# Kernel tuning notes

Hardware: AMD Instinct MI355X
Metric: run time of the kernel (lower is better)

Reference implementation:

```python
import jax, jax.numpy as jnp
import numpy as np


def pairwise_dist(x):
    # Euclidean cdist via the expansion trick; grad-safe sqrt (0 grad at 0, like torch).
    sq = jnp.sum(x * x, axis=1)
    d2 = sq[:, None] + sq[None, :] - 2.0 * (x @ x.T)
    d2 = jnp.maximum(d2, 0.0)
    pos = d2 > 0
    return jnp.where(pos, jnp.sqrt(jnp.where(pos, d2, 1.0)), 0.0)


def knn_mask(dist, k):
    # per-row ascending sort; skip index 0 (self), take next k neighbors
    idx = jnp.argsort(dist, axis=1)[:, 1:k + 1]            # [N, k]
    n = dist.shape[0]
    return jnp.zeros_like(dist).at[jnp.arange(n)[:, None], idx].set(1.0)


def setup_inputs() -> dict:
    key = jax.random.key(0)
    k1, k2 = jax.random.split(key)
    N, D, K = 8192, 64, 12
    latent = jax.random.normal(k1, (N, D), dtype=jnp.float32)
    latent_norm = jnp.ones((), dtype=jnp.float32)
    X = jax.random.normal(k2, (N, D), dtype=jnp.float32)
    dist_X = pairwise_dist(X)
    pair_mask_X = knn_mask(dist_X, K)
    return {"latent": latent, "latent_norm": latent_norm,
            "dist_X": dist_X, "pair_mask_X": pair_mask_X, "k": K}


def reference(latent, latent_norm, dist_X, pair_mask_X, k):
    n = latent.shape[0]
    dist_Z = pairwise_dist(latent) / latent_norm
    pair_mask_Z = knn_mask(dist_Z, k)

    mask_diff = pair_mask_Z - pair_mask_X
    matched = (n * k - jnp.sum(mask_diff != 0) * 0.5) / (n * k)

    # match_edges == 'symmetric'
    sig1 = dist_X * pair_mask_X
    sig1_2 = dist_Z * pair_mask_X
    distance1_2 = jnp.sum(jnp.square(sig1 - sig1_2))
    sig2 = dist_Z * pair_mask_Z
    sig2_1 = dist_X * pair_mask_Z
    distance2_1 = jnp.sum(jnp.square(sig2_1 - sig2))
    distance = distance1_2 + distance2_1
    return (distance, matched, distance1_2, distance2_1)
```

## Files before the change

kernel.cpp:

```cpp
#include <hip/hip_runtime.h>
#include <stdint.h>

constexpr int NPTS = 8192;
constexpr int DIM  = 64;
constexpr int KNN  = 12;

constexpr int RT = 64;
constexpr int CT = 64;
constexpr int CS = 4;
constexpr int STRIPE = NPTS / CS;
constexpr int NCHUNK = STRIPE / CT;
constexpr int AS_STRIDE = RT + 4;
constexpr int BS_STRIDE = CT + 4;

constexpr unsigned long long SENTINEL = 0xFFFFFFFFFFFFFFFFull;

__global__ void init_out(float* out) {
  if (threadIdx.x < 4) out[threadIdx.x] = 0.0f;
}

__global__ __launch_bounds__(256) void sq_kernel(const float* __restrict__ latent,
                                                 float* __restrict__ sq) {
  int i = blockIdx.x * 256 + threadIdx.x;
  const float4* p = reinterpret_cast<const float4*>(latent + (size_t)i * DIM);
  float s = 0.f;
#pragma unroll
  for (int t = 0; t < DIM / 4; ++t) {
    float4 v = p[t];
    s += v.x * v.x + v.y * v.y + v.z * v.z + v.w * v.w;
  }
  sq[i] = s;
}

__device__ __forceinline__ void topk_insert(unsigned long long cand,
                                            unsigned long long pk[KNN]) {
#pragma unroll
  for (int s = KNN - 1; s >= 0; --s) {
    bool belongs = cand < pk[s];
    bool shift = (s > 0) && (cand < pk[s - 1]);
    unsigned long long nv = shift ? pk[s - 1] : cand;
    if (belongs) pk[s] = nv;
  }
}

__global__ __launch_bounds__(256, 2) void dz_main(
    const float* __restrict__ latent, const float* __restrict__ latent_norm,
    const float* __restrict__ dist_X, const float* __restrict__ mask_X,
    const float* __restrict__ sq, unsigned long long* __restrict__ topk_ws,
    float* __restrict__ d_out) {
  __shared__ float As[DIM * AS_STRIDE];
  __shared__ float Bs[DIM * BS_STRIDE];
  __shared__ unsigned long long buf[RT * CT];
  __shared__ int   cnt[RT];
  __shared__ float thr[RT];
  __shared__ float sqA[RT];
  __shared__ float sqB[CT];
  __shared__ float red[256];

  const int tid = threadIdx.x;
  const int tile = blockIdx.x / CS;
  const int split = blockIdx.x % CS;
  const int ib = tile * RT;
  const int jb0 = split * STRIPE;

  const float invnorm = 1.0f / latent_norm[0];

#pragma unroll
  for (int i = 0; i < (RT * DIM) / 256; ++i) {
    int flat = i * 256 + tid;
    int k = flat & (DIM - 1);
    int r = flat >> 6;
    As[k * AS_STRIDE + r] = latent[(size_t)(ib + r) * DIM + k];
  }
  if (tid < RT) { sqA[tid] = sq[ib + tid]; thr[tid] = 3.4e38f; }

  unsigned long long pk[KNN];
#pragma unroll
  for (int t = 0; t < KNN; ++t) pk[t] = SENTINEL;

  const int tr = tid >> 4, tc = tid & 15;
  const int r0 = tr * 4, c0 = tc * 4;
  float acc1 = 0.f;

  for (int ch = 0; ch < NCHUNK; ++ch) {
    const int jb = jb0 + ch * CT;
    __syncthreads();
#pragma unroll
    for (int i = 0; i < (CT * DIM) / 256; ++i) {
      int flat = i * 256 + tid;
      int k = flat & (DIM - 1);
      int c = flat >> 6;
      Bs[k * BS_STRIDE + c] = latent[(size_t)(jb + c) * DIM + k];
    }
    if (tid < CT) sqB[tid] = sq[jb + tid];
    if (tid < RT) cnt[tid] = 0;
    __syncthreads();

    float4 dxv[4], mxv[4];
#pragma unroll
    for (int ri = 0; ri < 4; ++ri) {
      size_t base = (size_t)(ib + r0 + ri) * NPTS + jb + c0;
      dxv[ri] = *reinterpret_cast<const float4*>(dist_X + base);
      mxv[ri] = *reinterpret_cast<const float4*>(mask_X + base);
    }

    float acc[4][4];
#pragma unroll
    for (int a = 0; a < 4; ++a)
#pragma unroll
      for (int b = 0; b < 4; ++b) acc[a][b] = 0.f;

#pragma unroll 8
    for (int k = 0; k < DIM; ++k) {
      float4 av = *reinterpret_cast<const float4*>(&As[k * AS_STRIDE + r0]);
      float4 bv = *reinterpret_cast<const float4*>(&Bs[k * BS_STRIDE + c0]);
      float aa[4] = {av.x, av.y, av.z, av.w};
      float bb[4] = {bv.x, bv.y, bv.z, bv.w};
#pragma unroll
      for (int ri = 0; ri < 4; ++ri)
#pragma unroll
        for (int ci = 0; ci < 4; ++ci) acc[ri][ci] += aa[ri] * bb[ci];
    }

#pragma unroll
    for (int ri = 0; ri < 4; ++ri) {
      const int r = r0 + ri;
      const int gi = ib + r;
      const float t_thr = thr[r];
      float dxa[4] = {dxv[ri].x, dxv[ri].y, dxv[ri].z, dxv[ri].w};
      float mxa[4] = {mxv[ri].x, mxv[ri].y, mxv[ri].z, mxv[ri].w};
#pragma unroll
      for (int ci = 0; ci < 4; ++ci) {
        const int j = jb + c0 + ci;
        float d2 = sqA[r] + sqB[c0 + ci] - 2.0f * acc[ri][ci];
        float d2c = fmaxf(d2, 0.0f);
        float dz = (d2c > 0.0f) ? sqrtf(d2c) * invnorm : 0.0f;
        float diff = dxa[ci] - dz;
        acc1 += mxa[ci] * diff * diff;
        if (d2c < t_thr && j != gi) {
          int pos = atomicAdd(&cnt[r], 1);
          buf[r * CT + pos] =
              ((unsigned long long)__float_as_uint(d2c) << 32) | (unsigned)j;
        }
      }
    }
    __syncthreads();

    if (tid < RT) {
      int n = cnt[tid];
      for (int t = 0; t < n; ++t) {
        unsigned long long cand = buf[tid * CT + t];
        if (cand < pk[KNN - 1]) topk_insert(cand, pk);
      }
      thr[tid] = __uint_as_float((unsigned)(pk[KNN - 1] >> 32));
    }
  }

  if (tid < RT) {
    size_t base = ((size_t)(ib + tid) * CS + split) * KNN;
#pragma unroll
    for (int t = 0; t < KNN; ++t) topk_ws[base + t] = pk[t];
  }

  red[tid] = acc1;
  __syncthreads();
  for (int s = 128; s > 0; s >>= 1) {
    if (tid < s) red[tid] += red[tid + s];
    __syncthreads();
  }
  if (tid == 0) {
    atomicAdd(&d_out[2], red[0]);
    atomicAdd(&d_out[0], red[0]);
  }
}

__global__ __launch_bounds__(256) void finalize_kernel(
    const float* __restrict__ latent_norm, const float* __restrict__ dist_X,
    const float* __restrict__ mask_X,
    const unsigned long long* __restrict__ topk_ws, float* __restrict__ d_out) {
  __shared__ float red[256];
  const int tid = threadIdx.x;
  const int gi = blockIdx.x * 256 + tid;
  const float invnorm = 1.0f / latent_norm[0];

  unsigned long long pk[KNN];
#pragma unroll
  for (int t = 0; t < KNN; ++t) pk[t] = SENTINEL;

  const unsigned long long* src = topk_ws + (size_t)gi * CS * KNN;
  for (int t = 0; t < CS * KNN; ++t) {
    unsigned long long cand = src[t];
    if (cand < pk[KNN - 1]) topk_insert(cand, pk);
  }

  float acc2 = 0.f, accc = 0.f;
#pragma unroll
  for (int t = 0; t < KNN; ++t) {
    unsigned j = (unsigned)(pk[t] & 0xFFFFFFFFull);
    float d2 = __uint_as_float((unsigned)(pk[t] >> 32));
    float dz = (d2 > 0.0f) ? sqrtf(d2) * invnorm : 0.0f;
    float dxv = dist_X[(size_t)gi * NPTS + j];
    float mxv = mask_X[(size_t)gi * NPTS + j];
    float diff = dxv - dz;
    acc2 += diff * diff;
    accc += mxv;
  }

  red[tid] = acc2;
  __syncthreads();
  for (int s = 128; s > 0; s >>= 1) {
    if (tid < s) red[tid] += red[tid + s];
    __syncthreads();
  }
  float racc2 = red[0];
  __syncthreads();
  red[tid] = accc;
  __syncthreads();
  for (int s = 128; s > 0; s >>= 1) {
    if (tid < s) red[tid] += red[tid + s];
    __syncthreads();
  }
  if (tid == 0) {
    atomicAdd(&d_out[3], racc2);
    atomicAdd(&d_out[0], racc2);
    atomicAdd(&d_out[1], red[0] * (1.0f / ((float)NPTS * (float)KNN)));
  }
}

extern "C" void kernel_launch(void* const* d_in, const int* in_sizes, int n_in,
                              void* d_out, int out_size, void* d_ws,
                              size_t ws_size, hipStream_t stream) {
  const float* latent      = (const float*)d_in[0];
  const float* latent_norm = (const float*)d_in[1];
  const float* dist_X      = (const float*)d_in[2];
  const float* mask_X      = (const float*)d_in[3];
  float* out = (float*)d_out;

  float* sq = (float*)d_ws;
  unsigned long long* topk =
      (unsigned long long*)((char*)d_ws + NPTS * sizeof(float));

  init_out<<<1, 64, 0, stream>>>(out);
  sq_kernel<<<NPTS / 256, 256, 0, stream>>>(latent, sq);
  dz_main<<<(NPTS / RT) * CS, 256, 0, stream>>>(latent, latent_norm, dist_X,
                                                mask_X, sq, topk, out);
  finalize_kernel<<<NPTS / 256, 256, 0, stream>>>(latent_norm, dist_X, mask_X,
                                                  topk, out);
}
```

Before: 674.3 us.

## Use split-bf16 MFMA for Gram tile and skip dist_X loads where mask is zero

Replaces the FP32 scalar-FMA Gram computation with MFMA 16x16x32 bf16 instructions. Each value is split into high and low bf16 parts and three products are accumulated to keep near-FP32 accuracy. The loop is re-mapped to wave-level 32x32 subtiles, and LDS becomes row-major bf16 storage. It also reads mask_X per element and loads dist_X only where the mask is nonzero, which cuts most of the dense dist_X traffic. Risks: the split-bf16 error could reorder near-tied neighbours, and mask loads are now scalar rather than float4.

```diff
diff --git a/kernel.cpp b/kernel.cpp
--- a/kernel.cpp
+++ b/kernel.cpp
@@ -10,10 +10,20 @@
 constexpr int CS = 4;
 constexpr int STRIPE = NPTS / CS;
 constexpr int NCHUNK = STRIPE / CT;
-constexpr int AS_STRIDE = RT + 4;
-constexpr int BS_STRIDE = CT + 4;
+constexpr int LSTR = 72;
 
 constexpr unsigned long long SENTINEL = 0xFFFFFFFFFFFFFFFFull;
+
+typedef short bf16x8 __attribute__((ext_vector_type(8)));
+typedef float f32x4  __attribute__((ext_vector_type(4)));
+
+__device__ __forceinline__ unsigned short f2bf(float x) {
+  unsigned u = __float_as_uint(x);
+  return (unsigned short)((u + 0x7FFFu + ((u >> 16) & 1u)) >> 16);
+}
+__device__ __forceinline__ float bf2f(unsigned short h) {
+  return __uint_as_float(((unsigned)h) << 16);
+}
 
 __global__ void init_out(float* out) {
   if (threadIdx.x < 4) out[threadIdx.x] = 0.0f;
@@ -48,8 +58,8 @@
     const float* __restrict__ dist_X, const float* __restrict__ mask_X,
     const float* __restrict__ sq, unsigned long long* __restrict__ topk_ws,
     float* __restrict__ d_out) {
-  __shared__ float As[DIM * AS_STRIDE];
-  __shared__ float Bs[DIM * BS_STRIDE];
+  __shared__ unsigned short Ah[RT * LSTR], Al[RT * LSTR];
+  __shared__ unsigned short Bh[CT * LSTR], Bl[CT * LSTR];
   __shared__ unsigned long long buf[RT * CT];
   __shared__ int   cnt[RT];
   __shared__ float thr[RT];
@@ -63,14 +73,27 @@
   const int ib = tile * RT;
   const int jb0 = split * STRIPE;
 
+  const int wid = tid >> 6;
+  const int lane = tid & 63;
+  const int quad = lane >> 4;
+  const int l16 = lane & 15;
+  const int wr = wid >> 1;
+  const int wc = wid & 1;
+
   const float invnorm = 1.0f / latent_norm[0];
 
 #pragma unroll
-  for (int i = 0; i < (RT * DIM) / 256; ++i) {
+  for (int i = 0; i < (RT * DIM) / (256 * 4); ++i) {
     int flat = i * 256 + tid;
-    int k = flat & (DIM - 1);
-    int r = flat >> 6;
-    As[k * AS_STRIDE + r] = latent[(size_t)(ib + r) * DIM + k];
+    int r = flat >> 4, kq = flat & 15;
+    float4 v = *reinterpret_cast<const float4*>(latent + (size_t)(ib + r) * DIM + kq * 4);
+    ushort4 h, l;
+    h.x = f2bf(v.x); l.x = f2bf(v.x - bf2f(h.x));
+    h.y = f2bf(v.y); l.y = f2bf(v.y - bf2f(h.y));
+    h.z = f2bf(v.z); l.z = f2bf(v.z - bf2f(h.z));
+    h.w = f2bf(v.w); l.w = f2bf(v.w - bf2f(h.w));
+    *reinterpret_cast<ushort4*>(&Ah[r * LSTR + kq * 4]) = h;
+    *reinterpret_cast<ushort4*>(&Al[r * LSTR + kq * 4]) = l;
   }
   if (tid < RT) { sqA[tid] = sq[ib + tid]; thr[tid] = 3.4e38f; }
 
@@ -78,69 +101,90 @@
 #pragma unroll
   for (int t = 0; t < KNN; ++t) pk[t] = SENTINEL;
 
-  const int tr = tid >> 4, tc = tid & 15;
-  const int r0 = tr * 4, c0 = tc * 4;
   float acc1 = 0.f;
 
   for (int ch = 0; ch < NCHUNK; ++ch) {
     const int jb = jb0 + ch * CT;
     __syncthreads();
-#pragma unroll
-    for (int i = 0; i < (CT * DIM) / 256; ++i) {
+
+#pragma unroll
+    for (int i = 0; i < (CT * DIM) / (256 * 4); ++i) {
       int flat = i * 256 + tid;
-      int k = flat & (DIM - 1);
-      int c = flat >> 6;
-      Bs[k * BS_STRIDE + c] = latent[(size_t)(jb + c) * DIM + k];
+      int c = flat >> 4, kq = flat & 15;
+      float4 v = *reinterpret_cast<const float4*>(latent + (size_t)(jb + c) * DIM + kq * 4);
+      ushort4 h, l;
+      h.x = f2bf(v.x); l.x = f2bf(v.x - bf2f(h.x));
+      h.y = f2bf(v.y); l.y = f2bf(v.y - bf2f(h.y));
+      h.z = f2bf(v.z); l.z = f2bf(v.z - bf2f(h.z));
+      h.w = f2bf(v.w); l.w = f2bf(v.w - bf2f(h.w));
+      *reinterpret_cast<ushort4*>(&Bh[c * LSTR + kq * 4]) = h;
+      *reinterpret_cast<ushort4*>(&Bl[c * LSTR + kq * 4]) = l;
     }
     if (tid < CT) sqB[tid] = sq[jb + tid];
     if (tid < RT) cnt[tid] = 0;
     __syncthreads();
 
-    float4 dxv[4], mxv[4];
-#pragma unroll
-    for (int ri = 0; ri < 4; ++ri) {
-      size_t base = (size_t)(ib + r0 + ri) * NPTS + jb + c0;
-      dxv[ri] = *reinterpret_cast<const float4*>(dist_X + base);
-      mxv[ri] = *reinterpret_cast<const float4*>(mask_X + base);
-    }
-
-    float acc[4][4];
-#pragma unroll
-    for (int a = 0; a < 4; ++a)
-#pragma unroll
-      for (int b = 0; b < 4; ++b) acc[a][b] = 0.f;
-
-#pragma unroll 8
-    for (int k = 0; k < DIM; ++k) {
-      float4 av = *reinterpret_cast<const float4*>(&As[k * AS_STRIDE + r0]);
-      float4 bv = *reinterpret_cast<const float4*>(&Bs[k * BS_STRIDE + c0]);
-      float aa[4] = {av.x, av.y, av.z, av.w};
-      float bb[4] = {bv.x, bv.y, bv.z, bv.w};
-#pragma unroll
-      for (int ri = 0; ri < 4; ++ri)
-#pragma unroll
-        for (int ci = 0; ci < 4; ++ci) acc[ri][ci] += aa[ri] * bb[ci];
-    }
-
-#pragma unroll
-    for (int ri = 0; ri < 4; ++ri) {
-      const int r = r0 + ri;
-      const int gi = ib + r;
-      const float t_thr = thr[r];
-      float dxa[4] = {dxv[ri].x, dxv[ri].y, dxv[ri].z, dxv[ri].w};
-      float mxa[4] = {mxv[ri].x, mxv[ri].y, mxv[ri].z, mxv[ri].w};
-#pragma unroll
-      for (int ci = 0; ci < 4; ++ci) {
-        const int j = jb + c0 + ci;
-        float d2 = sqA[r] + sqB[c0 + ci] - 2.0f * acc[ri][ci];
-        float d2c = fmaxf(d2, 0.0f);
-        float dz = (d2c > 0.0f) ? sqrtf(d2c) * invnorm : 0.0f;
-        float diff = dxa[ci] - dz;
-        acc1 += mxa[ci] * diff * diff;
-        if (d2c < t_thr && j != gi) {
-          int pos = atomicAdd(&cnt[r], 1);
-          buf[r * CT + pos] =
-              ((unsigned long long)__float_as_uint(d2c) << 32) | (unsigned)j;
+    f32x4 acc[2][2];
+#pragma unroll
+    for (int rb = 0; rb < 2; ++rb)
+#pragma unroll
+      for (int cb = 0; cb < 2; ++cb) acc[rb][cb] = (f32x4){0.f, 0.f, 0.f, 0.f};
+
+#pragma unroll
+    for (int kk = 0; kk < 2; ++kk) {
+      const int ko = kk * 32 + quad * 8;
+      bf16x8 ah[2], al[2], bh[2], bl[2];
+#pragma unroll
+      for (int rb = 0; rb < 2; ++rb) {
+        int row = wr * 32 + rb * 16 + l16;
+        ah[rb] = *reinterpret_cast<const bf16x8*>(&Ah[row * LSTR + ko]);
+        al[rb] = *reinterpret_cast<const bf16x8*>(&Al[row * LSTR + ko]);
+      }
+#pragma unroll
+      for (int cb = 0; cb < 2; ++cb) {
+        int col = wc * 32 + cb * 16 + l16;
+        bh[cb] = *reinterpret_cast<const bf16x8*>(&Bh[col * LSTR + ko]);
+        bl[cb] = *reinterpret_cast<const bf16x8*>(&Bl[col * LSTR + ko]);
+      }
+#pragma unroll
+      for (int rb = 0; rb < 2; ++rb)
+#pragma unroll
+        for (int cb = 0; cb < 2; ++cb) {
+          acc[rb][cb] = __builtin_amdgcn_mfma_f32_16x16x32_bf16(ah[rb], bh[cb], acc[rb][cb], 0, 0, 0);
+          acc[rb][cb] = __builtin_amdgcn_mfma_f32_16x16x32_bf16(ah[rb], bl[cb], acc[rb][cb], 0, 0, 0);
+          acc[rb][cb] = __builtin_amdgcn_mfma_f32_16x16x32_bf16(al[rb], bh[cb], acc[rb][cb], 0, 0, 0);
+        }
+    }
+
+#pragma unroll
+    for (int rb = 0; rb < 2; ++rb) {
+#pragma unroll
+      for (int cb = 0; cb < 2; ++cb) {
+        const int row0 = wr * 32 + rb * 16 + quad * 4;
+        const int col_l = wc * 32 + cb * 16 + l16;
+        const int gj = jb + col_l;
+        const float sqb = sqB[col_l];
+        float mv[4];
+#pragma unroll
+        for (int r = 0; r < 4; ++r)
+          mv[r] = mask_X[(size_t)(ib + row0 + r) * NPTS + gj];
+#pragma unroll
+        for (int r = 0; r < 4; ++r) {
+          const int rl = row0 + r;
+          const int gi = ib + rl;
+          float d2 = sqA[rl] + sqb - 2.0f * acc[rb][cb][r];
+          float d2c = fmaxf(d2, 0.0f);
+          float dz = (d2c > 0.0f) ? sqrtf(d2c) * invnorm : 0.0f;
+          if (mv[r] != 0.0f) {
+            float dx = dist_X[(size_t)gi * NPTS + gj];
+            float diff = dx - dz;
+            acc1 += mv[r] * diff * diff;
+          }
+          if (d2c < thr[rl] && gj != gi) {
+            int pos = atomicAdd(&cnt[rl], 1);
+            buf[rl * CT + pos] =
+                ((unsigned long long)__float_as_uint(d2c) << 32) | (unsigned)gj;
+          }
         }
       }
     }
```

Result: no change. 676.7 us (+0.4%).
